# Kernel tuning notes

Measured on AMD Instinct MI355X. Metric: run time of the kernel, lower is better.

The kernel has to match this reference:

```python
import jax, jax.numpy as jnp
import numpy as np

N, E, F, H, L, G = 200000, 400000, 128, 128, 3, 4096
BN_EPS = 1e-5


def setup_inputs() -> dict:
    key = jax.random.key(0)
    ks = jax.random.split(key, 8)
    x = jax.random.normal(ks[0], (N, F), dtype=jnp.float32)
    edge_index = jax.random.randint(ks[1], (2, E), 0, N, dtype=jnp.int64)
    batch = jnp.sort(jax.random.randint(ks[2], (N,), 0, G, dtype=jnp.int64))
    s = 1.0 / np.sqrt(H)
    W_in = (jax.random.normal(ks[3], (F, H), jnp.float32) * s)
    b_in = jnp.zeros((H,), jnp.float32)
    W_conv = (jax.random.normal(ks[4], (L, H, H), jnp.float32) * s)
    b_conv = jnp.zeros((L, H), jnp.float32)
    gamma = jnp.ones((L, H), jnp.float32)
    beta = jnp.zeros((L, H), jnp.float32)
    W_out = (jax.random.normal(ks[5], (H, H), jnp.float32) * s)
    b_out = jnp.zeros((H,), jnp.float32)
    return dict(x=x, W_in=W_in, b_in=b_in, W_conv=W_conv, b_conv=b_conv,
                gamma=gamma, beta=beta, W_out=W_out, b_out=b_out,
                edge_index=edge_index, batch=batch)


def reference(x, W_in, b_in, W_conv, b_conv, gamma, beta, W_out, b_out,
              edge_index, batch):
    # --- GCN normalization (PyG GCNConv with self-loops, symmetric norm) ---
    loops = jnp.arange(N, dtype=edge_index.dtype)
    row = jnp.concatenate([edge_index[0], loops])  # source nodes
    col = jnp.concatenate([edge_index[1], loops])  # target nodes
    deg = jax.ops.segment_sum(jnp.ones_like(col, x.dtype), col, num_segments=N)
    dinv = jnp.where(deg > 0, jax.lax.rsqrt(deg), 0.0)
    norm = dinv[row] * dinv[col]                   # [E+N]

    h = x @ W_in + b_in                            # [N, H]
    for i in range(L):
        # GCNConv: linear -> gather -> normalize -> scatter-add -> bias
        msg = (h @ W_conv[i])[row] * norm[:, None]
        hn = jax.ops.segment_sum(msg, col, num_segments=N) + b_conv[i]
        # BatchNorm1d (batch statistics, as in training) + ReLU, residual
        mu = hn.mean(axis=0)
        var = hn.var(axis=0)
        hn = (hn - mu) * jax.lax.rsqrt(var + BN_EPS) * gamma[i] + beta[i]
        h = h + jax.nn.relu(hn)

    # global_mean_pool over batch assignment
    ssum = jax.ops.segment_sum(h, batch, num_segments=G)
    cnt = jax.ops.segment_sum(jnp.ones((N,), h.dtype), batch, num_segments=G)
    g = ssum / jnp.clip(cnt, 1.0)[:, None]         # [G, H]
    return g @ W_out + b_out
```

## Files before the change

### kernel.cpp

```cpp
#include <hip/hip_runtime.h>

#define NN 200000
#define NE 400000
#define HD 128
#define NL 3
#define NG 4096
#define BN_EPS 1e-5f

#define OFF_DINV  0UL
#define OFF_H     800000UL
#define OFF_U     103200000UL
#define OFF_ACC   205600000UL
#define OFF_POOL  308000000UL
#define OFF_GSTART 310097152UL
#define OFF_CSUM  310113540UL
#define OFF_CSQ   310115076UL
#define OFF_SCALE 310116612UL
#define OFF_SHIFT 310117124UL
#define OFF_CNTI  310117636UL
#define OFF_OFFS  310917636UL
#define OFF_CUR   311717652UL
#define OFF_SRCS  312517652UL
#define OFF_BSUM  314117652UL

#define SCAN_B 196

typedef __attribute__((ext_vector_type(8))) short v8s;
typedef __attribute__((ext_vector_type(4))) float v4f;
typedef __attribute__((ext_vector_type(4))) unsigned short v4u;
typedef __attribute__((ext_vector_type(8))) unsigned short v8u;

__device__ inline unsigned short f_to_bf_rne(float f) {
    unsigned u = __float_as_uint(f);
    return (unsigned short)((u + 0x7fffu + ((u >> 16) & 1u)) >> 16);
}

__device__ inline float bf_to_f(unsigned short a) {
    return __uint_as_float(((unsigned)a) << 16);
}

__device__ inline v4f bf4_to_f(v4u a) {
    v4f r;
    r[0] = bf_to_f(a[0]); r[1] = bf_to_f(a[1]);
    r[2] = bf_to_f(a[2]); r[3] = bf_to_f(a[3]);
    return r;
}

__global__ void count_deg_i(const int* __restrict__ col, int* __restrict__ cnt) {
    int e = blockIdx.x * blockDim.x + threadIdx.x;
    if (e < NE) atomicAdd(&cnt[col[e]], 1);
}

__global__ void finalize_dinv(const int* __restrict__ cnt, float* __restrict__ dinv) {
    int i = blockIdx.x * blockDim.x + threadIdx.x;
    if (i < NN) dinv[i] = rsqrtf((float)(cnt[i] + 1));
}

__global__ void scan_phase1(const int* __restrict__ cnt, int* __restrict__ bsum) {
    __shared__ int sh[256];
    int b = blockIdx.x, t = threadIdx.x;
    int base = b * 1024 + t * 4;
    int s = 0;
#pragma unroll
    for (int j = 0; j < 4; ++j) if (base + j < NN) s += cnt[base + j];
    sh[t] = s;
    __syncthreads();
    for (int st = 128; st > 0; st >>= 1) {
        if (t < st) sh[t] += sh[t + st];
        __syncthreads();
    }
    if (t == 0) bsum[b] = sh[0];
}

__global__ void scan_phase2(int* __restrict__ bsum, int* __restrict__ offs) {
    if (threadIdx.x == 0) {
        int run = 0;
        for (int i = 0; i < SCAN_B; ++i) { int v = bsum[i]; bsum[i] = run; run += v; }
        offs[NN] = NE;
    }
}

__global__ void scan_phase3(const int* __restrict__ cnt, const int* __restrict__ bsum,
                            int* __restrict__ offs) {
    __shared__ int sh[256];
    int b = blockIdx.x, t = threadIdx.x;
    int base = b * 1024 + t * 4;
    int v[4];
    int s = 0;
#pragma unroll
    for (int j = 0; j < 4; ++j) { v[j] = (base + j < NN) ? cnt[base + j] : 0; s += v[j]; }
    sh[t] = s;
    __syncthreads();
    for (int st = 1; st < 256; st <<= 1) {
        int x = (t >= st) ? sh[t - st] : 0;
        __syncthreads();
        sh[t] += x;
        __syncthreads();
    }
    int run = sh[t] - s + bsum[b];
#pragma unroll
    for (int j = 0; j < 4; ++j) {
        if (base + j < NN) { offs[base + j] = run; run += v[j]; }
    }
}

__global__ void fill_csr(const int* __restrict__ row, const int* __restrict__ col,
                         const int* __restrict__ offs, int* __restrict__ cur,
                         int* __restrict__ srcs) {
    int e = blockIdx.x * blockDim.x + threadIdx.x;
    if (e >= NE) return;
    int c = col[e];
    int p = offs[c] + atomicAdd(&cur[c], 1);
    srcs[p] = row[e];
}

__device__ inline void cvt_split(float f, short& hi, short& lo) {
    unsigned u = __float_as_uint(f);
    unsigned rh = (u + 0x7fffu + ((u >> 16) & 1u)) >> 16;
    hi = (short)rh;
    float fh = __uint_as_float(rh << 16);
    float d = f - fh;
    unsigned u2 = __float_as_uint(d);
    unsigned rl = (u2 + 0x7fffu + ((u2 >> 16) & 1u)) >> 16;
    lo = (short)rl;
}

#define GEMM_BLOCKS 512
template <bool ADD_BIAS, bool SCALE_DINV, bool FUSE_BN, bool A_BF16>
__launch_bounds__(1024, 4)
__global__ void gemm_mfma(void* __restrict__ Av, const float* __restrict__ W,
                          const float* __restrict__ bias, const float* __restrict__ dinv,
                          const float* __restrict__ bnscale, const float* __restrict__ bnshift,
                          const unsigned short* __restrict__ bnacc,
                          unsigned short* __restrict__ O, int M) {
    __shared__ short Wh[HD * HD];
    __shared__ short Wlo[HD * HD];

    {
        int c = threadIdx.x >> 3;
        int eighth = threadIdx.x & 7;
#pragma unroll
        for (int g8 = 0; g8 < 2; ++g8) {
            int G = eighth * 2 + g8;
            v8s h8, l8;
#pragma unroll
            for (int j = 0; j < 8; ++j) {
                float f = W[(G * 8 + j) * HD + c];
                short hi, lo;
                cvt_split(f, hi, lo);
                h8[j] = hi; l8[j] = lo;
            }
            int off = c * HD + (G ^ (c & 7)) * 8;
            *(v8s*)&Wh[off] = h8;
            *(v8s*)&Wlo[off] = l8;
        }
    }
    __syncthreads();

    int wave = threadIdx.x >> 6;
    int lane = threadIdx.x & 63;
    int m = lane & 15;
    int q = lane >> 4;

    for (int task = blockIdx.x; task * 256 < M; task += GEMM_BLOCKS) {
        int rbase = task * 256 + wave * 16;
        if (rbase >= M) continue;

        v8s ah[4], al[4];
#pragma unroll
        for (int kc = 0; kc < 4; ++kc) {
            if (!A_BF16) {
                const float* Ar = (const float*)Av + (size_t)(rbase + m) * HD;
                float4 x0 = *(const float4*)(Ar + kc * 32 + q * 8);
                float4 x1 = *(const float4*)(Ar + kc * 32 + q * 8 + 4);
                float xs[8] = {x0.x, x0.y, x0.z, x0.w, x1.x, x1.y, x1.z, x1.w};
                v8s h8, l8;
#pragma unroll
                for (int j = 0; j < 8; ++j) {
                    short hi, lo;
                    cvt_split(xs[j], hi, lo);
                    h8[j] = hi; l8[j] = lo;
                }
                ah[kc] = h8; al[kc] = l8;
            } else {
                unsigned short* Ar = (unsigned short*)Av + (size_t)(rbase + m) * HD;
                v8u a8 = *(const v8u*)(Ar + kc * 32 + q * 8);
                if (FUSE_BN) {
                    v8u y8 = *(const v8u*)(bnacc + (size_t)(rbase + m) * HD + kc * 32 + q * 8);
                    const float* scp = bnscale + kc * 32 + q * 8;
                    const float* sfp = bnshift + kc * 32 + q * 8;
                    v8u o8;
#pragma unroll
                    for (int j = 0; j < 8; ++j) {
                        float hn = bf_to_f(a8[j]) +
                                   fmaxf(fmaf(bf_to_f(y8[j]), scp[j], sfp[j]), 0.f);
                        o8[j] = f_to_bf_rne(hn);
                    }
                    *(v8u*)(Ar + kc * 32 + q * 8) = o8;
                    a8 = o8;
                }
                ah[kc] = (v8s)a8;
            }
        }

        v4f acc[8];
#pragma unroll
        for (int ct = 0; ct < 8; ++ct) acc[ct] = (v4f){0.f, 0.f, 0.f, 0.f};

#pragma unroll
        for (int kc = 0; kc < 4; ++kc) {
#pragma unroll
            for (int ct = 0; ct < 8; ++ct) {
                int c = ct * 16 + m;
                int off = c * HD + (((kc * 4 + q) ^ (c & 7)) * 8);
                v8s bh = *(const v8s*)&Wh[off];
                v8s bl = *(const v8s*)&Wlo[off];
                acc[ct] = __builtin_amdgcn_mfma_f32_16x16x32_bf16(ah[kc], bh, acc[ct], 0, 0, 0);
                if (!A_BF16)
                    acc[ct] = __builtin_amdgcn_mfma_f32_16x16x32_bf16(al[kc], bh, acc[ct], 0, 0, 0);
                acc[ct] = __builtin_amdgcn_mfma_f32_16x16x32_bf16(ah[kc], bl, acc[ct], 0, 0, 0);
            }
        }

        float dv[4];
#pragma unroll
        for (int reg = 0; reg < 4; ++reg)
            dv[reg] = SCALE_DINV ? dinv[rbase + q * 4 + reg] : 1.0f;
#pragma unroll
        for (int ct = 0; ct < 8; ++ct) {
            int colb = ct * 16 + m;
            float bb = ADD_BIAS ? bias[colb] : 0.0f;
#pragma unroll
            for (int reg = 0; reg < 4; ++reg) {
                int rr = rbase + q * 4 + reg;
                float v = acc[ct][reg] + bb;
                if (SCALE_DINV) v *= dv[reg];
                O[(size_t)rr * HD + colb] = f_to_bf_rne(v);
            }
        }
    }
}

#define GATHER_BLOCKS 1024
__global__ void gather_bn(const int* __restrict__ offs, const int* __restrict__ srcs,
                          const unsigned short* __restrict__ u, const float* __restrict__ dinv,
                          unsigned short* __restrict__ acc,
                          float* __restrict__ colsum, float* __restrict__ colsumsq) {
    const v8u* u8p = (const v8u*)u;
    v8u* acc8 = (v8u*)acc;
    int n = threadIdx.x >> 4;
    int q = threadIdx.x & 15;
    v4f t1a = (v4f){0.f, 0.f, 0.f, 0.f}, t1b = t1a;
    v4f t2a = t1a, t2b = t1a;

    for (int node = blockIdx.x * 16 + n; node < NN; node += GATHER_BLOCKS * 16) {
        v8u s8 = u8p[(size_t)node * 16 + q];
        v4f sa = bf4_to_f((v4u){s8[0], s8[1], s8[2], s8[3]});
        v4f sb = bf4_to_f((v4u){s8[4], s8[5], s8[6], s8[7]});
        int k = offs[node];
        int k1 = offs[node + 1];
        for (; k + 2 <= k1; k += 2) {
            int s0 = srcs[k], s1 = srcs[k + 1];
            v8u a8 = u8p[(size_t)s0 * 16 + q];
            v8u b8 = u8p[(size_t)s1 * 16 + q];
            sa += bf4_to_f((v4u){a8[0], a8[1], a8[2], a8[3]});
            sb += bf4_to_f((v4u){a8[4], a8[5], a8[6], a8[7]});
            sa += bf4_to_f((v4u){b8[0], b8[1], b8[2], b8[3]});
            sb += bf4_to_f((v4u){b8[4], b8[5], b8[6], b8[7]});
        }
        if (k < k1) {
            v8u a8 = u8p[(size_t)srcs[k] * 16 + q];
            sa += bf4_to_f((v4u){a8[0], a8[1], a8[2], a8[3]});
            sb += bf4_to_f((v4u){a8[4], a8[5], a8[6], a8[7]});
        }
        float d = dinv[node];
        sa *= d; sb *= d;
        v8u o8;
        o8[0] = f_to_bf_rne(sa[0]); o8[1] = f_to_bf_rne(sa[1]);
        o8[2] = f_to_bf_rne(sa[2]); o8[3] = f_to_bf_rne(sa[3]);
        o8[4] = f_to_bf_rne(sb[0]); o8[5] = f_to_bf_rne(sb[1]);
        o8[6] = f_to_bf_rne(sb[2]); o8[7] = f_to_bf_rne(sb[3]);
        acc8[(size_t)node * 16 + q] = o8;
        v4f ra = bf4_to_f((v4u){o8[0], o8[1], o8[2], o8[3]});
        v4f rb = bf4_to_f((v4u){o8[4], o8[5], o8[6], o8[7]});
        t1a += ra; t1b += rb;
        t2a += ra * ra; t2b += rb * rb;
    }

    __shared__ float sh1[16][HD];
    __shared__ float sh2[16][HD];
    *(v4f*)&sh1[n][q * 8] = t1a;
    *(v4f*)&sh1[n][q * 8 + 4] = t1b;
    *(v4f*)&sh2[n][q * 8] = t2a;
    *(v4f*)&sh2[n][q * 8 + 4] = t2b;
    __syncthreads();
    if (threadIdx.x < HD) {
        int c = threadIdx.x;
        float a1 = 0.f, a2 = 0.f;
#pragma unroll
        for (int i = 0; i < 16; ++i) { a1 += sh1[i][c]; a2 += sh2[i][c]; }
        atomicAdd(&colsum[c], a1);
        atomicAdd(&colsumsq[c], a2);
    }
}

__global__ void bn_finalize(const float* __restrict__ colsum, const float* __restrict__ colsumsq,
                            const float* __restrict__ gamma, const float* __restrict__ beta,
                            float* __restrict__ scale, float* __restrict__ shift) {
    int c = threadIdx.x;
    float invn = 1.0f / (float)NN;
    float m = colsum[c] * invn;
    float v = colsumsq[c] * invn - m * m;
    float sc = gamma[c] * rsqrtf(v + BN_EPS);
    scale[c] = sc;
    shift[c] = beta[c] - m * sc;
}

__global__ void group_bounds(const int* __restrict__ batch, int* __restrict__ gstart) {
    int g = blockIdx.x * blockDim.x + threadIdx.x;
    if (g > NG) return;
    if (g == NG) { gstart[NG] = NN; return; }
    int lo = 0, hi = NN;
    while (lo < hi) {
        int mid = (lo + hi) >> 1;
        if (batch[mid] < g) lo = mid + 1; else hi = mid;
    }
    gstart[g] = lo;
}

__launch_bounds__(128)
__global__ void pool_bn_mean(const unsigned short* __restrict__ acc,
                             const unsigned short* __restrict__ h,
                             const float* __restrict__ scale, const float* __restrict__ shift,
                             const int* __restrict__ gstart, float* __restrict__ pool) {
    int g = blockIdx.x;
    int c = threadIdx.x;
    float sc = scale[c], sf = shift[c];
    int s = gstart[g], e = gstart[g + 1];
    float a = 0.f;
    for (int r = s; r < e; ++r) {
        float yv = bf_to_f(acc[(size_t)r * HD + c]);
        float y = fmaxf(fmaf(yv, sc, sf), 0.f);
        a += bf_to_f(h[(size_t)r * HD + c]) + y;
    }
    float ic = 1.0f / fmaxf((float)(e - s), 1.0f);
    pool[(size_t)g * HD + c] = a * ic;
}

__launch_bounds__(128)
__global__ void out_gemm(const float* __restrict__ pool,
                         const float* __restrict__ Wout, const float* __restrict__ bout,
                         float* __restrict__ out) {
    __shared__ float hb[HD];
    int g = blockIdx.x;
    int c = threadIdx.x;
    hb[c] = pool[(size_t)g * HD + c];
    __syncthreads();
    float o = bout[c];
#pragma unroll 8
    for (int k = 0; k < HD; ++k) o = fmaf(hb[k], Wout[k * HD + c], o);
    out[(size_t)g * HD + c] = o;
}

extern "C" void kernel_launch(void* const* d_in, const int* in_sizes, int n_in,
                              void* d_out, int out_size, void* d_ws, size_t ws_size,
                              hipStream_t stream) {
    const float* x      = (const float*)d_in[0];
    const float* W_in   = (const float*)d_in[1];
    const float* b_in   = (const float*)d_in[2];
    const float* W_conv = (const float*)d_in[3];
    const float* gamma  = (const float*)d_in[5];
    const float* beta   = (const float*)d_in[6];
    const float* W_out  = (const float*)d_in[7];
    const float* b_out  = (const float*)d_in[8];
    const int*   edge   = (const int*)d_in[9];
    const int*   batch  = (const int*)d_in[10];
    float* out = (float*)d_out;

    char* ws = (char*)d_ws;
    float* dinv   = (float*)(ws + OFF_DINV);
    unsigned short* h   = (unsigned short*)(ws + OFF_H);
    unsigned short* u   = (unsigned short*)(ws + OFF_U);
    unsigned short* acc = (unsigned short*)(ws + OFF_ACC);
    float* pool   = (float*)(ws + OFF_POOL);
    int*   gstart = (int*)(ws + OFF_GSTART);
    float* csum   = (float*)(ws + OFF_CSUM);
    float* csq    = (float*)(ws + OFF_CSQ);
    float* scale  = (float*)(ws + OFF_SCALE);
    float* shift  = (float*)(ws + OFF_SHIFT);
    int*   cnti   = (int*)(ws + OFF_CNTI);
    int*   offs   = (int*)(ws + OFF_OFFS);
    int*   cur    = (int*)(ws + OFF_CUR);
    int*   srcs   = (int*)(ws + OFF_SRCS);
    int*   bsum   = (int*)(ws + OFF_BSUM);

    const int* row = edge;
    const int* col = edge + NE;

    hipMemsetAsync(ws + OFF_CSUM, 0, OFF_SHIFT + 512 - OFF_CSUM, stream);
    hipMemsetAsync(ws + OFF_CNTI, 0, OFF_SRCS - OFF_CNTI, stream);

    count_deg_i<<<(NE + 255) / 256, 256, 0, stream>>>(col, cnti);
    finalize_dinv<<<(NN + 255) / 256, 256, 0, stream>>>(cnti, dinv);
    scan_phase1<<<SCAN_B, 256, 0, stream>>>(cnti, bsum);
    scan_phase2<<<1, 64, 0, stream>>>(bsum, offs);
    scan_phase3<<<SCAN_B, 256, 0, stream>>>(cnti, bsum, offs);
    fill_csr<<<(NE + 255) / 256, 256, 0, stream>>>(row, col, offs, cur, srcs);
    group_bounds<<<(NG + 256) / 256, 256, 0, stream>>>(batch, gstart);

    gemm_mfma<true, false, false, false><<<GEMM_BLOCKS, 1024, 0, stream>>>(
        (void*)x, W_in, b_in, nullptr, nullptr, nullptr, nullptr, h, NN);

    for (int l = 0; l < NL; ++l) {
        if (l == 0) {
            gemm_mfma<false, true, false, true><<<GEMM_BLOCKS, 1024, 0, stream>>>(
                h, W_conv + (size_t)l * HD * HD, nullptr, dinv,
                nullptr, nullptr, nullptr, u, NN);
        } else {
            gemm_mfma<false, true, true, true><<<GEMM_BLOCKS, 1024, 0, stream>>>(
                h, W_conv + (size_t)l * HD * HD, nullptr, dinv,
                scale, shift, acc, u, NN);
        }
        gather_bn<<<GATHER_BLOCKS, 256, 0, stream>>>(
            offs, srcs, u, dinv, acc, csum + l * HD, csq + l * HD);
        bn_finalize<<<1, HD, 0, stream>>>(
            csum + l * HD, csq + l * HD, gamma + l * HD, beta + l * HD, scale, shift);
    }

    pool_bn_mean<<<NG, 128, 0, stream>>>(acc, h, scale, shift, gstart, pool);
    out_gemm<<<NG, 128, 0, stream>>>(pool, W_out, b_out, out);
}
```

Measured before the change: 639.3 us.

## Fold small launches: merge dinv/scan phases and inline BN finalize into consumers

```diff
diff --git a/kernel.cpp b/kernel.cpp
--- a/kernel.cpp
+++ b/kernel.cpp
@@ -15,8 +15,6 @@
 #define OFF_GSTART 310097152UL
 #define OFF_CSUM  310113540UL
 #define OFF_CSQ   310115076UL
-#define OFF_SCALE 310116612UL
-#define OFF_SHIFT 310117124UL
 #define OFF_CNTI  310117636UL
 #define OFF_OFFS  310917636UL
 #define OFF_CUR   311717652UL
@@ -51,11 +49,6 @@
     if (e < NE) atomicAdd(&cnt[col[e]], 1);
 }
 
-__global__ void finalize_dinv(const int* __restrict__ cnt, float* __restrict__ dinv) {
-    int i = blockIdx.x * blockDim.x + threadIdx.x;
-    if (i < NN) dinv[i] = rsqrtf((float)(cnt[i] + 1));
-}
-
 __global__ void scan_phase1(const int* __restrict__ cnt, int* __restrict__ bsum) {
     __shared__ int sh[256];
     int b = blockIdx.x, t = threadIdx.x;
@@ -72,18 +65,20 @@
     if (t == 0) bsum[b] = sh[0];
 }
 
-__global__ void scan_phase2(int* __restrict__ bsum, int* __restrict__ offs) {
-    if (threadIdx.x == 0) {
-        int run = 0;
-        for (int i = 0; i < SCAN_B; ++i) { int v = bsum[i]; bsum[i] = run; run += v; }
-        offs[NN] = NE;
-    }
-}
-
 __global__ void scan_phase3(const int* __restrict__ cnt, const int* __restrict__ bsum,
-                            int* __restrict__ offs) {
+                            int* __restrict__ offs, float* __restrict__ dinv) {
     __shared__ int sh[256];
+    __shared__ int shb[256];
     int b = blockIdx.x, t = threadIdx.x;
+
+    shb[t] = (t < b && t < SCAN_B) ? bsum[t] : 0;
+    __syncthreads();
+    for (int st = 128; st > 0; st >>= 1) {
+        if (t < st) shb[t] += shb[t + st];
+        __syncthreads();
+    }
+    int base_sum = shb[0];
+
     int base = b * 1024 + t * 4;
     int v[4];
     int s = 0;
@@ -97,11 +92,16 @@
         sh[t] += x;
         __syncthreads();
     }
-    int run = sh[t] - s + bsum[b];
+    int run = sh[t] - s + base_sum;
 #pragma unroll
     for (int j = 0; j < 4; ++j) {
-        if (base + j < NN) { offs[base + j] = run; run += v[j]; }
-    }
+        if (base + j < NN) {
+            offs[base + j] = run;
+            dinv[base + j] = rsqrtf((float)(v[j] + 1));
+            run += v[j];
+        }
+    }
+    if (b == 0 && t == 0) offs[NN] = NE;
 }
 
 __global__ void fill_csr(const int* __restrict__ row, const int* __restrict__ col,
@@ -130,11 +130,14 @@
 __launch_bounds__(1024, 4)
 __global__ void gemm_mfma(void* __restrict__ Av, const float* __restrict__ W,
                           const float* __restrict__ bias, const float* __restrict__ dinv,
-                          const float* __restrict__ bnscale, const float* __restrict__ bnshift,
+                          const float* __restrict__ csum, const float* __restrict__ csq,
+                          const float* __restrict__ gamma, const float* __restrict__ beta,
                           const unsigned short* __restrict__ bnacc,
                           unsigned short* __restrict__ O, int M) {
     __shared__ short Wh[HD * HD];
     __shared__ short Wlo[HD * HD];
+    __shared__ float bnsc[HD];
+    __shared__ float bnsf[HD];
 
     {
         int c = threadIdx.x >> 3;
@@ -154,6 +157,15 @@
             *(v8s*)&Wh[off] = h8;
             *(v8s*)&Wlo[off] = l8;
         }
+    }
+    if (FUSE_BN && threadIdx.x < HD) {
+        int c = threadIdx.x;
+        float invn = 1.0f / (float)NN;
+        float mmean = csum[c] * invn;
+        float var = csq[c] * invn - mmean * mmean;
+        float sc = gamma[c] * rsqrtf(var + BN_EPS);
+        bnsc[c] = sc;
+        bnsf[c] = beta[c] - mmean * sc;
     }
     __syncthreads();
 
@@ -187,8 +199,8 @@
                 v8u a8 = *(const v8u*)(Ar + kc * 32 + q * 8);
                 if (FUSE_BN) {
                     v8u y8 = *(const v8u*)(bnacc + (size_t)(rbase + m) * HD + kc * 32 + q * 8);
-                    const float* scp = bnscale + kc * 32 + q * 8;
-                    const float* sfp = bnshift + kc * 32 + q * 8;
+                    const float* scp = bnsc + kc * 32 + q * 8;
+                    const float* sfp = bnsf + kc * 32 + q * 8;
                     v8u o8;
 #pragma unroll
                     for (int j = 0; j < 8; ++j) {
@@ -241,7 +253,7 @@
     }
 }
 
-#define GATHER_BLOCKS 1024
+#define GATHER_BLOCKS 2048
 __global__ void gather_bn(const int* __restrict__ offs, const int* __restrict__ srcs,
                           const unsigned short* __restrict__ u, const float* __restrict__ dinv,
                           unsigned short* __restrict__ acc,
@@ -304,18 +316,6 @@
     }
 }
 
-__global__ void bn_finalize(const float* __restrict__ colsum, const float* __restrict__ colsumsq,
-                            const float* __restrict__ gamma, const float* __restrict__ beta,
-                            float* __restrict__ scale, float* __restrict__ shift) {
-    int c = threadIdx.x;
-    float invn = 1.0f / (float)NN;
-    float m = colsum[c] * invn;
-    float v = colsumsq[c] * invn - m * m;
-    float sc = gamma[c] * rsqrtf(v + BN_EPS);
-    scale[c] = sc;
-    shift[c] = beta[c] - m * sc;
-}
-
 __global__ void group_bounds(const int* __restrict__ batch, int* __restrict__ gstart) {
     int g = blockIdx.x * blockDim.x + threadIdx.x;
     if (g > NG) return;
@@ -331,11 +331,16 @@
 __launch_bounds__(128)
 __global__ void pool_bn_mean(const unsigned short* __restrict__ acc,
                              const unsigned short* __restrict__ h,
-                             const float* __restrict__ scale, const float* __restrict__ shift,
+                             const float* __restrict__ csum, const float* __restrict__ csq,
+                             const float* __restrict__ gamma, const float* __restrict__ beta,
                              const int* __restrict__ gstart, float* __restrict__ pool) {
     int g = blockIdx.x;
     int c = threadIdx.x;
-    float sc = scale[c], sf = shift[c];
+    float invn = 1.0f / (float)NN;
+    float mmean = csum[c] * invn;
+    float var = csq[c] * invn - mmean * mmean;
+    float sc = gamma[c] * rsqrtf(var + BN_EPS);
+    float sf = beta[c] - mmean * sc;
     int s = gstart[g], e = gstart[g + 1];
     float a = 0.f;
     for (int r = s; r < e; ++r) {
@@ -386,8 +391,6 @@
     int*   gstart = (int*)(ws + OFF_GSTART);
     float* csum   = (float*)(ws + OFF_CSUM);
     float* csq    = (float*)(ws + OFF_CSQ);
-    float* scale  = (float*)(ws + OFF_SCALE);
-    float* shift  = (float*)(ws + OFF_SHIFT);
     int*   cnti   = (int*)(ws + OFF_CNTI);
     int*   offs   = (int*)(ws + OFF_OFFS);
     int*   cur    = (int*)(ws + OFF_CUR);
@@ -397,36 +400,37 @@
     const int* row = edge;
     const int* col = edge + NE;
 
-    hipMemsetAsync(ws + OFF_CSUM, 0, OFF_SHIFT + 512 - OFF_CSUM, stream);
+    hipMemsetAsync(ws + OFF_CSUM, 0, OFF_CNTI - OFF_CSUM, stream);
     hipMemsetAsync(ws + OFF_CNTI, 0, OFF_SRCS - OFF_CNTI, stream);
 
     count_deg_i<<<(NE + 255) / 256, 256, 0, stream>>>(col, cnti);
-    finalize_dinv<<<(NN + 255) / 256, 256, 0, stream>>>(cnti, dinv);
     scan_phase1<<<SCAN_B, 256, 0, stream>>>(cnti, bsum);
-    scan_phase2<<<1, 64, 0, stream>>>(bsum, offs);
-    scan_phase3<<<SCAN_B, 256, 0, stream>>>(cnti, bsum, offs);
+    scan_phase3<<<SCAN_B, 256, 0, stream>>>(cnti, bsum, offs, dinv);
     fill_csr<<<(NE + 255) / 256, 256, 0, stream>>>(row, col, offs, cur, srcs);
     group_bounds<<<(NG + 256) / 256, 256, 0, stream>>>(batch, gstart);
 
     gemm_mfma<true, false, false, false><<<GEMM_BLOCKS, 1024, 0, stream>>>(
-        (void*)x, W_in, b_in, nullptr, nullptr, nullptr, nullptr, h, NN);
+        (void*)x, W_in, b_in, nullptr, nullptr, nullptr, nullptr, nullptr,
+        nullptr, h, NN);
 
     for (int l = 0; l < NL; ++l) {
         if (l == 0) {
             gemm_mfma<false, true, false, true><<<GEMM_BLOCKS, 1024, 0, stream>>>(
                 h, W_conv + (size_t)l * HD * HD, nullptr, dinv,
-                nullptr, nullptr, nullptr, u, NN);
+                nullptr, nullptr, nullptr, nullptr, nullptr, u, NN);
         } else {
             gemm_mfma<false, true, true, true><<<GEMM_BLOCKS, 1024, 0, stream>>>(
                 h, W_conv + (size_t)l * HD * HD, nullptr, dinv,
-                scale, shift, acc, u, NN);
+                csum + (l - 1) * HD, csq + (l - 1) * HD,
+                gamma + (size_t)(l - 1) * HD, beta + (size_t)(l - 1) * HD,
+                acc, u, NN);
         }
         gather_bn<<<GATHER_BLOCKS, 256, 0, stream>>>(
             offs, srcs, u, dinv, acc, csum + l * HD, csq + l * HD);
-        bn_finalize<<<1, HD, 0, stream>>>(
-            csum + l * HD, csq + l * HD, gamma + l * HD, beta + l * HD, scale, shift);
-    }
-
-    pool_bn_mean<<<NG, 128, 0, stream>>>(acc, h, scale, shift, gstart, pool);
+    }
+
+    pool_bn_mean<<<NG, 128, 0, stream>>>(
+        acc, h, csum + (NL - 1) * HD, csq + (NL - 1) * HD,
+        gamma + (size_t)(NL - 1) * HD, beta + (size_t)(NL - 1) * HD, gstart, pool);
     out_gemm<<<NG, 128, 0, stream>>>(pool, W_out, b_out, out);
 }
```

Result: slower. 697.6 us (+9.1%).
